# Optimization experiments

Measured on AMD Instinct MI355X. Metric: run time of the kernel, lower is better.

## Reference

```python
import jax, jax.numpy as jnp
import numpy as np
import math

N, E, O, C, KD, KEYD = 50000, 800000, 4, 64, 16, 128


def setup_inputs() -> dict:
    key = jax.random.key(0)
    ks = jax.random.split(key, 10)
    x = jax.random.normal(ks[0], (N, O, C), jnp.float32)
    kernel_basis = jax.random.normal(ks[1], (E, O, KD), jnp.float32)
    fiber_kernel_basis = jax.random.normal(ks[2], (O, O, KD), jnp.float32)
    edge_index = jax.random.randint(ks[3], (2, E), 0, N, jnp.int32)
    # nn.Linear default init ~ U(-1/sqrt(fan_in), 1/sqrt(fan_in)); scaled normal is fine as data
    kernel_W = jax.random.normal(ks[4], (C, KD), jnp.float32) / math.sqrt(KD)        # kernel: Linear(kernel_dim -> in_channels)
    fiber_kernel_W = jax.random.normal(ks[5], (C, KD), jnp.float32) / math.sqrt(KD)  # depthwise: in*out/groups = C
    key_W = jax.random.normal(ks[6], (KEYD, C), jnp.float32) / math.sqrt(C)
    key_b = jnp.zeros((KEYD,), jnp.float32)
    query_W = jax.random.normal(ks[7], (KEYD, C), jnp.float32) / math.sqrt(C)
    query_b = jnp.zeros((KEYD,), jnp.float32)
    bias = jnp.zeros((C,), jnp.float32)
    return {"x": x, "kernel_basis": kernel_basis, "fiber_kernel_basis": fiber_kernel_basis,
            "edge_index": edge_index, "kernel_W": kernel_W, "fiber_kernel_W": fiber_kernel_W,
            "key_W": key_W, "key_b": key_b, "query_W": query_W, "query_b": query_b, "bias": bias}


def reference(x, kernel_basis, fiber_kernel_basis, edge_index, kernel_W, fiber_kernel_W,
              key_W, key_b, query_W, query_b, bias):
    src = edge_index[0]
    dst = edge_index[1]
    n = x.shape[0]
    # per-edge spatial kernel: [E,O,KD] @ [KD,C] -> [E,O,C]
    k = jnp.einsum('eok,ck->eoc', kernel_basis, kernel_W)
    message = x[src] * k                                       # [E,O,C]
    # scatter-softmax attention over incoming edges of each target node
    keys = jnp.einsum('noc,kc->nok', x, key_W) + key_b        # [N,O,KEYD]
    queries = jnp.einsum('noc,kc->nok', x, query_W) + query_b
    logits = jnp.sum(keys[src] * queries[dst], axis=-1, keepdims=True) / math.sqrt(KEYD)  # [E,O,1]
    e = jnp.exp(logits - jnp.max(logits))                      # global-max stabilization, as in source
    denom = jax.ops.segment_sum(e, dst, num_segments=n) + 1e-6 # [N,O,1]
    att = e / denom[dst]
    message = message * att
    # scatter-add aggregation into target nodes
    x1 = jax.ops.segment_sum(message, dst, num_segments=n)     # [N,O,C]
    # fiber (orientation) mixing kernel: [O,O,KD] @ [KD,C] -> [O,O,C]
    fk = jnp.einsum('pok,ck->poc', fiber_kernel_basis, fiber_kernel_W)
    x2 = jnp.einsum('boc,poc->bpc', x1, fk) / fk.shape[-2]
    return x2 + bias
```

## Files before the change

### kernel.cpp

```cpp
#include <hip/hip_runtime.h>
#include <math.h>

#define NN 50000
#define EE 800000
#define OO 4
#define CC 64
#define KDD 16
#define KEYDD 128
#define CH 8

typedef float v2f __attribute__((ext_vector_type(2)));

__device__ __forceinline__ float wave_red_sum(float v) {
  int x;
  x = __builtin_amdgcn_update_dpp(0, __float_as_int(v), 0x111, 0xf, 0xf, false);
  v += __int_as_float(x);
  x = __builtin_amdgcn_update_dpp(0, __float_as_int(v), 0x112, 0xf, 0xf, false);
  v += __int_as_float(x);
  x = __builtin_amdgcn_update_dpp(0, __float_as_int(v), 0x114, 0xf, 0xf, false);
  v += __int_as_float(x);
  x = __builtin_amdgcn_update_dpp(0, __float_as_int(v), 0x118, 0xf, 0xf, false);
  v += __int_as_float(x);
  x = __builtin_amdgcn_update_dpp(0, __float_as_int(v), 0x142, 0xa, 0xf, false);
  v += __int_as_float(x);
  x = __builtin_amdgcn_update_dpp(0, __float_as_int(v), 0x143, 0xc, 0xf, false);
  v += __int_as_float(x);
  return __int_as_float(__builtin_amdgcn_readlane(__float_as_int(v), 63));
}

__device__ __forceinline__ float exp2_fast(float x) {
  float r;
  asm("v_exp_f32 %0, %1" : "=v"(r) : "v"(x));
  return r;
}

__device__ __forceinline__ void red4(float q0, float q1, float q2, float q3,
                                     float& p0, float& p1, float& p2, float& p3) {
  asm("s_nop 1\n\tv_permlane32_swap_b32 %0, %1" : "+v"(q0), "+v"(q1));
  float ra = q0 + q1;
  asm("s_nop 1\n\tv_permlane32_swap_b32 %0, %1" : "+v"(q2), "+v"(q3));
  float rb = q2 + q3;
  asm("s_nop 1\n\t"
      "v_add_f32_dpp %0, %0, %0 row_shr:1 row_mask:0xf bank_mask:0xf bound_ctrl:0\n\t"
      "v_add_f32_dpp %1, %1, %1 row_shr:1 row_mask:0xf bank_mask:0xf bound_ctrl:0\n\t"
      "v_add_f32_dpp %0, %0, %0 row_shr:2 row_mask:0xf bank_mask:0xf bound_ctrl:0\n\t"
      "v_add_f32_dpp %1, %1, %1 row_shr:2 row_mask:0xf bank_mask:0xf bound_ctrl:0\n\t"
      "v_add_f32_dpp %0, %0, %0 row_shr:4 row_mask:0xf bank_mask:0xf bound_ctrl:0\n\t"
      "v_add_f32_dpp %1, %1, %1 row_shr:4 row_mask:0xf bank_mask:0xf bound_ctrl:0\n\t"
      "v_add_f32_dpp %0, %0, %0 row_shr:8 row_mask:0xf bank_mask:0xf bound_ctrl:0\n\t"
      "v_add_f32_dpp %1, %1, %1 row_shr:8 row_mask:0xf bank_mask:0xf bound_ctrl:0\n\t"
      "v_add_f32_dpp %0, %0, %0 row_bcast:15 row_mask:0xa bank_mask:0xf bound_ctrl:0\n\t"
      "v_add_f32_dpp %1, %1, %1 row_bcast:15 row_mask:0xa bank_mask:0xf bound_ctrl:0\n\t"
      "s_nop 0"
      : "+v"(ra), "+v"(rb));
  p0 = __int_as_float(__builtin_amdgcn_readlane(__float_as_int(ra), 31));
  p1 = __int_as_float(__builtin_amdgcn_readlane(__float_as_int(ra), 63));
  p2 = __int_as_float(__builtin_amdgcn_readlane(__float_as_int(rb), 31));
  p3 = __int_as_float(__builtin_amdgcn_readlane(__float_as_int(rb), 63));
}

__global__ void prep_kernel(const float* __restrict__ keyW, const float* __restrict__ keyB,
                            const float* __restrict__ qryW, const float* __restrict__ qryB,
                            const float* __restrict__ fkb, const float* __restrict__ fkw,
                            float* __restrict__ Mt, float* __restrict__ aVec,
                            float* __restrict__ bVec, float* __restrict__ c0,
                            float* __restrict__ fk) {
  __shared__ float qw[KEYDD * CC];
  __shared__ float kws[KEYDD * 4];
  int t = threadIdx.x, b = blockIdx.x;
  if (b < 16) {
    for (int i = t; i < KEYDD * CC; i += 256) qw[i] = qryW[i];
    for (int i = t; i < KEYDD * 4; i += 256) {
      int k = i >> 2, c1l = i & 3;
      kws[i] = keyW[k * CC + b * 4 + c1l];
    }
    __syncthreads();
    int c1l = t >> 6, c2 = t & 63;
    float s = 0.f;
    #pragma unroll 8
    for (int k = 0; k < KEYDD; ++k)
      s = fmaf(kws[k * 4 + c1l], qw[k * CC + c2], s);
    Mt[c2 * CC + b * 4 + c1l] = s;
  } else {
    if (t < CC) {
      float sa = 0.f, sb = 0.f;
      for (int k = 0; k < KEYDD; ++k) {
        sa = fmaf(keyB[k], qryW[k * CC + t], sa);
        sb = fmaf(qryB[k], keyW[k * CC + t], sb);
      }
      aVec[t] = sa; bVec[t] = sb;
    }
    if (t == 0) {
      float s = 0.f;
      for (int k = 0; k < KEYDD; ++k) s = fmaf(keyB[k], qryB[k], s);
      c0[0] = s;
    }
    for (int idx = t; idx < OO * OO * CC; idx += 256) {
      int p = idx >> 8, rem = idx & 255;
      int o = rem >> 6, c = rem & 63;
      float s = 0.f;
      #pragma unroll
      for (int kd = 0; kd < KDD; ++kd)
        s = fmaf(fkb[(p * OO + o) * KDD + kd], fkw[c * KDD + kd], s);
      fk[idx] = 0.25f * s;
    }
  }
}

__global__ void count_kernel(const int* __restrict__ ei, int* __restrict__ counts) {
  int e = blockIdx.x * 256 + threadIdx.x;
  if (e < EE) atomicAdd(&counts[ei[EE + e]], 1);
}

__global__ void scan1_kernel(const int* __restrict__ counts, int* __restrict__ incl,
                             int* __restrict__ bsum, int n) {
  __shared__ int buf[256];
  int t = threadIdx.x;
  int i = blockIdx.x * 256 + t;
  int v = (i < n) ? counts[i] : 0;
  buf[t] = v;
  __syncthreads();
  for (int off = 1; off < 256; off <<= 1) {
    int a = buf[t];
    int b2 = (t >= off) ? buf[t - off] : 0;
    __syncthreads();
    buf[t] = a + b2;
    __syncthreads();
  }
  if (i < n) incl[i] = buf[t];
  if (t == 255) bsum[blockIdx.x] = buf[255];
}
__global__ void scan2_kernel(const int* __restrict__ bsum, int* __restrict__ bbase, int nb) {
  __shared__ int buf[256];
  int t = threadIdx.x;
  int v = (t < nb) ? bsum[t] : 0;
  buf[t] = v;
  __syncthreads();
  for (int off = 1; off < 256; off <<= 1) {
    int a = buf[t];
    int b2 = (t >= off) ? buf[t - off] : 0;
    __syncthreads();
    buf[t] = a + b2;
    __syncthreads();
  }
  if (t < nb) bbase[t] = buf[t] - v;
}
__global__ void scan3_kernel(const int* __restrict__ counts, const int* __restrict__ incl,
                             const int* __restrict__ bbase, int* __restrict__ offsets, int n) {
  int i = blockIdx.x * 256 + threadIdx.x;
  if (i < n) {
    int oi = bbase[blockIdx.x] + incl[i];
    offsets[i] = oi - counts[i];
    if (i == n - 1) offsets[n] = oi;
  }
}

__global__ void fill_kernel(const int* __restrict__ ei, const int* __restrict__ offsets,
                            int* __restrict__ counts, long long* __restrict__ pairs) {
  int e = blockIdx.x * 256 + threadIdx.x;
  if (e < EE) {
    int d = ei[EE + e];
    int r = atomicSub(&counts[d], 1) - 1;
    int pos = offsets[d] + r;
    pairs[pos] = ((long long)ei[e] << 32) | (unsigned)e;
  }
}

__device__ __forceinline__ float kv_dot(const float* __restrict__ kb, int ej, int obase,
                                        float4 kw0, float4 kw1, float4 kw2, float4 kw3) {
  const float4* bp = reinterpret_cast<const float4*>(kb + ej * (OO * KDD) + obase);
  float4 b0 = bp[0], b1 = bp[1], b2 = bp[2], b3 = bp[3];
  v2f a0 = {0.f, 0.f}, a1 = {0.f, 0.f};
  #define P2(f4, i) (reinterpret_cast<const v2f*>(&(f4))[i])
  a0 = __builtin_elementwise_fma(P2(b0, 0), P2(kw0, 0), a0);
  a1 = __builtin_elementwise_fma(P2(b0, 1), P2(kw0, 1), a1);
  a0 = __builtin_elementwise_fma(P2(b1, 0), P2(kw1, 0), a0);
  a1 = __builtin_elementwise_fma(P2(b1, 1), P2(kw1, 1), a1);
  a0 = __builtin_elementwise_fma(P2(b2, 0), P2(kw2, 0), a0);
  a1 = __builtin_elementwise_fma(P2(b2, 1), P2(kw2, 1), a1);
  a0 = __builtin_elementwise_fma(P2(b3, 0), P2(kw3, 0), a0);
  a1 = __builtin_elementwise_fma(P2(b3, 1), P2(kw3, 1), a1);
  #undef P2
  v2f s = a0 + a1;
  return s.x + s.y;
}

__global__ __launch_bounds__(256, 4) void mega_kernel(
    const float* __restrict__ x, const float* __restrict__ Mt,
    const float* __restrict__ aVec, const float* __restrict__ bVec,
    const float* __restrict__ c0p, const float* __restrict__ kb,
    const float* __restrict__ kW, const int* __restrict__ offsets,
    const long long* __restrict__ pairs, const float* __restrict__ fkg,
    const float* __restrict__ bias, float* __restrict__ out) {
  __shared__ float x1[OO * CC];
  int n = blockIdx.x;
  int t = threadIdx.x;
  int o = __builtin_amdgcn_readfirstlane(t >> 6);
  int c = t & 63;
  const float scale2 = 0.12751541050862828f;
  int js = offsets[n], je = offsets[n + 1];
  int deg = je - js;
  int dm1 = deg - 1;

  long long prAll = 0;
  if (deg > 0) prAll = pairs[js + min(c, dm1)];

  int rowoff = __builtin_amdgcn_readfirstlane((n * OO + o) * CC);
  const float* xrow = x + rowoff;
  float ub0 = 0.f, ub1 = 0.f, ub2 = 0.f, ub3 = 0.f;
  #pragma unroll
  for (int q = 0; q < 16; ++q) {
    ub0 = fmaf(Mt[(4 * q + 0) * CC + c], xrow[4 * q + 0], ub0);
    ub1 = fmaf(Mt[(4 * q + 1) * CC + c], xrow[4 * q + 1], ub1);
    ub2 = fmaf(Mt[(4 * q + 2) * CC + c], xrow[4 * q + 2], ub2);
    ub3 = fmaf(Mt[(4 * q + 3) * CC + c], xrow[4 * q + 3], ub3);
  }
  float ubr = (((ub0 + ub1) + (ub2 + ub3)) + bVec[c]) * scale2;
  float xown = xrow[c];
  float base2 = (wave_red_sum(aVec[c] * xown) + c0p[0]) * scale2;

  const float4* kwp = reinterpret_cast<const float4*>(kW + c * KDD);
  float4 kw0 = kwp[0], kw1 = kwp[1], kw2 = kwp[2], kw3 = kwp[3];
  int obase = o * KDD;
  int voff = c << 2;

  int e_all = (int)((unsigned long long)prAll & 0xffffffffu);
  int s_all = (int)(prAll >> 32);

  float S = 0.f, acc = 0.f;
  int degc = min(deg, 64);

  #define GATHER(XV, CS)                                                       \
  {                                                                            \
    _Pragma("unroll")                                                          \
    for (int j = 0; j < CH; ++j) {                                             \
      int li = (CS) + j; li = (li < dm1) ? li : dm1;                           \
      int sj = __builtin_amdgcn_readlane(s_all, li);                           \
      const float* pj = x + (size_t)(sj * OO + o) * CC;                        \
      asm volatile("global_load_dword %0, %1, %2"                              \
                   : "=v"(XV[j]) : "v"(voff), "s"(pj));                        \
    }                                                                          \
  }
  #define SUB4(XV, CS, J0, CL)                                                 \
  {                                                                            \
    int la = (CS)+(J0)+0; la = (la < dm1) ? la : dm1;                          \
    int lb = (CS)+(J0)+1; lb = (lb < dm1) ? lb : dm1;                          \
    int lc2 = (CS)+(J0)+2; lc2 = (lc2 < dm1) ? lc2 : dm1;                      \
    int ld = (CS)+(J0)+3; ld = (ld < dm1) ? ld : dm1;                          \
    float kv0 = kv_dot(kb, __builtin_amdgcn_readlane(e_all, la), obase, kw0, kw1, kw2, kw3);  \
    float kv1 = kv_dot(kb, __builtin_amdgcn_readlane(e_all, lb), obase, kw0, kw1, kw2, kw3);  \
    float kv2 = kv_dot(kb, __builtin_amdgcn_readlane(e_all, lc2), obase, kw0, kw1, kw2, kw3); \
    float kv3 = kv_dot(kb, __builtin_amdgcn_readlane(e_all, ld), obase, kw0, kw1, kw2, kw3);  \
    float p0, p1, p2, p3;                                                      \
    red4(XV[(J0) + 0] * ubr, XV[(J0) + 1] * ubr,                               \
         XV[(J0) + 2] * ubr, XV[(J0) + 3] * ubr, p0, p1, p2, p3);              \
    float ev0 = ((J0) + 0 < (CL)) ? exp2_fast(p0) : 0.f;                       \
    float ev1 = ((J0) + 1 < (CL)) ? exp2_fast(p1) : 0.f;                       \
    float ev2 = ((J0) + 2 < (CL)) ? exp2_fast(p2) : 0.f;                       \
    float ev3 = ((J0) + 3 < (CL)) ? exp2_fast(p3) : 0.f;                       \
    S += (ev0 + ev1) + (ev2 + ev3);                                            \
    acc = fmaf(ev0 * kv0, XV[(J0) + 0], acc);                                  \
    acc = fmaf(ev1 * kv1, XV[(J0) + 1], acc);                                  \
    acc = fmaf(ev2 * kv2, XV[(J0) + 2], acc);                                  \
    acc = fmaf(ev3 * kv3, XV[(J0) + 3], acc);                                  \
  }
  #define COMPUTE(XV, CS, CL)                                                  \
    SUB4(XV, CS, 0, CL)                                                        \
    if ((CL) > 4) SUB4(XV, CS, 4, CL)

  if (degc > 0) {
    float xvA[CH], xvB[CH];
    GATHER(xvA, 0)
    int cs = 0;
    while (true) {
      int cl = degc - cs; if (cl > CH) cl = CH;
      bool hasNext = (cs + CH) < degc;
      asm volatile("s_waitcnt vmcnt(0)" ::: "memory");
      __builtin_amdgcn_sched_barrier(0);
      if (hasNext) GATHER(xvB, cs + CH)
      __builtin_amdgcn_sched_barrier(0);
      COMPUTE(xvA, cs, cl)
      if (!hasNext) break;
      cs += CH;
      cl = degc - cs; if (cl > CH) cl = CH;
      hasNext = (cs + CH) < degc;
      asm volatile("s_waitcnt vmcnt(0)" ::: "memory");
      __builtin_amdgcn_sched_barrier(0);
      if (hasNext) GATHER(xvA, cs + CH)
      __builtin_amdgcn_sched_barrier(0);
      COMPUTE(xvB, cs, cl)
      if (!hasNext) break;
      cs += CH;
    }
  }
  #undef COMPUTE
  #undef SUB4
  #undef GATHER

  for (int eidx = 64; eidx < deg; ++eidx) {
    long long pp = pairs[js + eidx];
    int sid = __builtin_amdgcn_readfirstlane((int)(pp >> 32));
    int eid = __builtin_amdgcn_readfirstlane((int)((unsigned long long)pp & 0xffffffffu));
    float xe = x[(size_t)(sid * OO + o) * CC + c];
    float p = wave_red_sum(xe * ubr);
    float ev = exp2_fast(p);
    float kv = kv_dot(kb, eid, obase, kw0, kw1, kw2, kw3);
    S += ev;
    acc = fmaf(ev * kv, xe, acc);
  }

  float invd = 1.0f / (S + 1e-6f * exp2_fast(-base2));
  x1[t] = acc * invd;
  __syncthreads();
  float s2s = 0.f;
  #pragma unroll
  for (int oo = 0; oo < OO; ++oo)
    s2s = fmaf(x1[oo * CC + c], fkg[o * (OO * CC) + oo * CC + c], s2s);
  out[(size_t)n * (OO * CC) + t] = s2s + bias[c];
}

extern "C" void kernel_launch(void* const* d_in, const int* in_sizes, int n_in,
                              void* d_out, int out_size, void* d_ws, size_t ws_size,
                              hipStream_t stream) {
  const float* x    = (const float*)d_in[0];
  const float* kb   = (const float*)d_in[1];
  const float* fkb  = (const float*)d_in[2];
  const int*   ei   = (const int*)d_in[3];
  const float* kW   = (const float*)d_in[4];
  const float* fkW  = (const float*)d_in[5];
  const float* keyW = (const float*)d_in[6];
  const float* keyB = (const float*)d_in[7];
  const float* qryW = (const float*)d_in[8];
  const float* qryB = (const float*)d_in[9];
  const float* bias = (const float*)d_in[10];
  float* out = (float*)d_out;

  const int NB = (NN + 255) / 256;

  float* wsf  = (float*)d_ws;
  float* Mt   = wsf;
  float* aVec = Mt + 4096;
  float* bVec = aVec + 64;
  float* c0   = bVec + 64;
  float* fk   = c0 + 64;
  long long* pairs = (long long*)(fk + 1024);
  int* counts    = (int*)(pairs + EE);
  int* offsets   = counts + NN;
  int* incl      = offsets + NN + 1;
  int* bsum      = incl + NN;
  int* bbase     = bsum + 256;

  hipMemsetAsync(counts, 0, (size_t)NN * sizeof(int), stream);

  prep_kernel<<<17, 256, 0, stream>>>(keyW, keyB, qryW, qryB, fkb, fkW, Mt, aVec, bVec, c0, fk);
  count_kernel<<<(EE + 255) / 256, 256, 0, stream>>>(ei, counts);
  scan1_kernel<<<NB, 256, 0, stream>>>(counts, incl, bsum, NN);
  scan2_kernel<<<1, 256, 0, stream>>>(bsum, bbase, NB);
  scan3_kernel<<<NB, 256, 0, stream>>>(counts, incl, bbase, offsets, NN);
  fill_kernel<<<(EE + 255) / 256, 256, 0, stream>>>(ei, offsets, counts, pairs);
  mega_kernel<<<NN, 256, 0, stream>>>(x, Mt, aVec, bVec, c0, kb, kW, offsets, pairs,
                                      fk, bias, out);
}
```

Measured before the change: 404.3 us.

## Triple-buffer neighbor feature gathers with partial vmcnt waits

The double-buffered gather loop over incoming edges becomes a three-buffer rotation. Two chunks of 8 source-row loads stay in flight, and each compute step waits only until at most 8 loads remain outstanding (vmcnt(8)) instead of draining all loads. This is meant to hide more gather latency for nodes with higher degree. It costs 8 more live VGPRs per thread, which may lower occupancy, and correctness depends on the vmcnt counts matching the issue order.

Measured after the change: 402.1 us. Within noise of the previous version (-0.6%).

```diff
diff --git a/kernel.cpp b/kernel.cpp
--- a/kernel.cpp
+++ b/kernel.cpp
@@ -241,6 +241,10 @@
                    : "=v"(XV[j]) : "v"(voff), "s"(pj));                        \
     }                                                                          \
   }
+  #define WAITK(HASN)                                                          \
+    if (HASN) { asm volatile("s_waitcnt vmcnt(8)" ::: "memory"); }             \
+    else      { asm volatile("s_waitcnt vmcnt(0)" ::: "memory"); }             \
+    __builtin_amdgcn_sched_barrier(0);
   #define SUB4(XV, CS, J0, CL)                                                 \
   {                                                                            \
     int la = (CS)+(J0)+0; la = (la < dm1) ? la : dm1;                          \
@@ -269,32 +273,42 @@
     if ((CL) > 4) SUB4(XV, CS, 4, CL)
 
   if (degc > 0) {
-    float xvA[CH], xvB[CH];
+    float xvA[CH], xvB[CH], xvC[CH];
+    asm volatile("s_waitcnt vmcnt(0)" ::: "memory");
+    __builtin_amdgcn_sched_barrier(0);
     GATHER(xvA, 0)
+    if (CH < degc) GATHER(xvB, CH)
     int cs = 0;
     while (true) {
       int cl = degc - cs; if (cl > CH) cl = CH;
-      bool hasNext = (cs + CH) < degc;
-      asm volatile("s_waitcnt vmcnt(0)" ::: "memory");
-      __builtin_amdgcn_sched_barrier(0);
-      if (hasNext) GATHER(xvB, cs + CH)
+      bool hasN1 = (cs + CH) < degc;
+      WAITK(hasN1)
+      if (cs + 2 * CH < degc) GATHER(xvC, cs + 2 * CH)
       __builtin_amdgcn_sched_barrier(0);
       COMPUTE(xvA, cs, cl)
-      if (!hasNext) break;
+      if (!hasN1) break;
       cs += CH;
       cl = degc - cs; if (cl > CH) cl = CH;
-      hasNext = (cs + CH) < degc;
-      asm volatile("s_waitcnt vmcnt(0)" ::: "memory");
-      __builtin_amdgcn_sched_barrier(0);
-      if (hasNext) GATHER(xvA, cs + CH)
+      hasN1 = (cs + CH) < degc;
+      WAITK(hasN1)
+      if (cs + 2 * CH < degc) GATHER(xvA, cs + 2 * CH)
       __builtin_amdgcn_sched_barrier(0);
       COMPUTE(xvB, cs, cl)
-      if (!hasNext) break;
+      if (!hasN1) break;
+      cs += CH;
+      cl = degc - cs; if (cl > CH) cl = CH;
+      hasN1 = (cs + CH) < degc;
+      WAITK(hasN1)
+      if (cs + 2 * CH < degc) GATHER(xvB, cs + 2 * CH)
+      __builtin_amdgcn_sched_barrier(0);
+      COMPUTE(xvC, cs, cl)
+      if (!hasN1) break;
       cs += CH;
     }
   }
   #undef COMPUTE
   #undef SUB4
+  #undef WAITK
   #undef GATHER
 
   for (int eidx = 64; eidx < deg; ++eidx) {
```
